# Kernel tuning notes

Measured on AMD Instinct MI355X. Metric: run time of the kernel, lower is better.

The kernel has to match this reference:

```python
import jax, jax.numpy as jnp
import numpy as np

N_NODES = 100000
DEG = 16
N_EDGES = N_NODES * DEG
D_FEAT = 64
HIDDEN = 64
K_RATIO = 0.5  # self.k
EPS = 1e-08


@jax.custom_vjp
def binary_step(x):
    return (x > 0.0).astype(x.dtype)

def _bs_fwd(x):
    return binary_step(x), x

def _bs_bwd(x, g):
    ax = jnp.abs(x)
    # BinaryStep surrogate gradient: 0 for |x|>1, 0.4 for 0.4<|x|<=1, else 2-4|x|
    add = jnp.where(ax > 1.0, 0.0, jnp.where(ax > 0.4, 0.4, 2.0 - 4.0 * ax))
    return (g * add,)

binary_step.defvjp(_bs_fwd, _bs_bwd)


def segment_softmax(v, seg, n):
    # torch.sparse.softmax(dim=1) == softmax over edges grouped by row id
    m = jax.ops.segment_max(v, seg, num_segments=n)
    e = jnp.exp(v - m[seg])
    s = jax.ops.segment_sum(e, seg, num_segments=n)
    return e / s[seg]


def setup_inputs() -> dict:
    key = jax.random.key(0)
    k1, k2, k3, k4, k5, k6, k7 = jax.random.split(key, 7)
    # coalesced edge list: rows sorted, (row,col) unique, every node has DEG edges
    rows = np.repeat(np.arange(N_NODES, dtype=np.int32), DEG)
    offs = np.tile(np.arange(1, DEG + 1, dtype=np.int32), N_NODES)
    cols = ((rows + offs) % N_NODES).reshape(N_NODES, DEG)
    cols = np.sort(cols, axis=1).reshape(-1).astype(np.int32)
    indices = jnp.asarray(np.stack([rows, cols]))  # [2, E]
    features = jax.random.normal(k1, (N_NODES, D_FEAT), dtype=jnp.float32)
    values = jax.random.uniform(k2, (N_EDGES,), dtype=jnp.float32, minval=0.1, maxval=1.0)
    U = jax.random.uniform(k3, (N_EDGES,), dtype=jnp.float32)
    gumbel = -jnp.log(-jnp.log(U + EPS) + EPS)  # Gumbel(0,1) noise (precomputed for determinism)
    in_dim = 2 * D_FEAT + 1
    w0 = jax.random.normal(k4, (HIDDEN, in_dim), dtype=jnp.float32) * (6.0 / (in_dim + HIDDEN)) ** 0.5
    b0 = jax.random.normal(k5, (HIDDEN,), dtype=jnp.float32) * 0.02
    w1 = jax.random.normal(k6, (1, HIDDEN), dtype=jnp.float32) * (6.0 / (HIDDEN + 1)) ** 0.5
    b1 = jax.random.normal(k7, (1,), dtype=jnp.float32) * 0.02
    return {"features": features, "values": values, "w0": w0, "b0": b0,
            "w1": w1, "b1": b1, "gumbel": gumbel, "indices": indices,
            "n_nodes": N_NODES, "temperature": 1}


def reference(features, values, w0, b0, w1, b1, gumbel, indices, n_nodes, temperature):
    rows = indices[0]
    cols = indices[1]
    # gather endpoint features + edge weight, 2-layer MLP -> scalar score per edge
    temp = jnp.concatenate([features[rows], features[cols], values[:, None]], axis=-1)  # [E, 2D+1]
    h = jax.nn.relu(temp @ w0.T + b0)          # [E, H]
    z = (h @ w1.T + b1).reshape(-1)            # [E]
    z = z / jnp.maximum(jnp.linalg.norm(z), 1e-12)  # F.normalize(dim=0)
    pi = segment_softmax(z, rows, n_nodes)           # sparse row softmax
    logits = (jnp.log(pi) + gumbel) / temperature    # gumbel_softmax_sample (training path)
    y = segment_softmax(logits, rows, n_nodes)
    # per-node top-k threshold masking
    counts = jax.ops.segment_sum(jnp.ones_like(rows), rows, num_segments=n_nodes)  # [N]
    k_edges = jnp.maximum(jnp.round(counts.astype(y.dtype) * K_RATIO).astype(rows.dtype), 1)
    val_sort_idx = jnp.argsort(-y)                                   # global descending sort
    idx_sort_idx = jnp.argsort(rows[val_sort_idx], stable=True)      # stable regroup by row
    scores_sorted = y[val_sort_idx][idx_sort_idx]                    # per-row descending scores
    rows_sorted = rows[val_sort_idx][idx_sort_idx]
    edge_start = jnp.concatenate([jnp.zeros((1,), counts.dtype), jnp.cumsum(counts[:-1])])
    edge_end = jnp.abs(edge_start + k_edges - 1)
    node_thre = scores_sorted[edge_end]          # k-th largest score per node
    thre_aug = node_thre[rows_sorted]            # == repeat_interleave(counts) since rows_sorted ascending
    mask = binary_step(scores_sorted - thre_aug + 1e-12)
    masked = mask * scores_sorted
    masked = masked[jnp.argsort(idx_sort_idx)]   # undo row regroup
    masked = masked[jnp.argsort(val_sort_idx)]   # undo value sort -> original edge order
    return masked
```

## Files before the change

### kernel.cpp

```cpp
#include <hip/hip_runtime.h>

#define N_NODES 100000
#define DEG 16
#define N_EDGES (N_NODES * DEG)
#define NT 64
#define NBLK2 ((N_NODES + NT - 1) / NT)
#define AB_TILES 2
#define NBLK_AB ((N_NODES + NT * AB_TILES - 1) / (NT * AB_TILES))

__global__ __launch_bounds__(256) void k_prep(const float* __restrict__ w0,
                                              float* __restrict__ w0T) {
    int id = blockIdx.x * 256 + threadIdx.x;
    if (id < 64 * 128) {
        int k = id >> 7, o = id & 127;
        w0T[k * 128 + o] = (o < 64) ? w0[o * 129 + k]
                                    : w0[(o - 64) * 129 + 64 + k];
    }
}

__global__ __launch_bounds__(256) void k_ab(const float* __restrict__ feat,
                                            const float* __restrict__ w0T,
                                            const float* __restrict__ b0,
                                            float* __restrict__ AB) {
    __shared__ float ws[64][128];
    __shared__ float fs[64][64];
    const int tid = threadIdx.x;
    const int to = tid & 31;
    const int tn = tid >> 5;

    for (int idx = tid; idx < 2048; idx += 256) {
        int k = idx >> 5, o4 = idx & 31;
        *(float4*)&ws[k][o4 * 4] = *(const float4*)&w0T[k * 128 + o4 * 4];
    }
    float4 bb = make_float4(0.f, 0.f, 0.f, 0.f);
    if (to < 16) bb = *(const float4*)(b0 + to * 4);

#define FMA16(ACCR, F4)                                   \
    ACCR[0] = fmaf(F4.x, w40.x, ACCR[0]);                 \
    ACCR[1] = fmaf(F4.x, w40.y, ACCR[1]);                 \
    ACCR[2] = fmaf(F4.x, w40.z, ACCR[2]);                 \
    ACCR[3] = fmaf(F4.x, w40.w, ACCR[3]);                 \
    ACCR[0] = fmaf(F4.y, w41.x, ACCR[0]);                 \
    ACCR[1] = fmaf(F4.y, w41.y, ACCR[1]);                 \
    ACCR[2] = fmaf(F4.y, w41.z, ACCR[2]);                 \
    ACCR[3] = fmaf(F4.y, w41.w, ACCR[3]);                 \
    ACCR[0] = fmaf(F4.z, w42.x, ACCR[0]);                 \
    ACCR[1] = fmaf(F4.z, w42.y, ACCR[1]);                 \
    ACCR[2] = fmaf(F4.z, w42.z, ACCR[2]);                 \
    ACCR[3] = fmaf(F4.z, w42.w, ACCR[3]);                 \
    ACCR[0] = fmaf(F4.w, w43.x, ACCR[0]);                 \
    ACCR[1] = fmaf(F4.w, w43.y, ACCR[1]);                 \
    ACCR[2] = fmaf(F4.w, w43.z, ACCR[2]);                 \
    ACCR[3] = fmaf(F4.w, w43.w, ACCR[3]);

#pragma unroll 1
    for (int tile = 0; tile < AB_TILES; ++tile) {
        const int n0 = blockIdx.x * (NT * AB_TILES) + tile * NT;
        if (n0 >= N_NODES) break;
        __syncthreads();
        for (int idx = tid; idx < 1024; idx += 256) {
            int flat = idx << 2;
            int nn = flat >> 6, k = flat & 63;
            int n = n0 + nn;
            float4 v = make_float4(0.f, 0.f, 0.f, 0.f);
            if (n < N_NODES) v = *(const float4*)(feat + (size_t)n * 64 + k);
            *(float4*)&fs[nn][k] = v;
        }
        __syncthreads();

        float acc[8][4];
#pragma unroll
        for (int a = 0; a < 8; ++a) {
            acc[a][0] = 0.f; acc[a][1] = 0.f; acc[a][2] = 0.f; acc[a][3] = 0.f;
        }
#pragma unroll 4
        for (int k4 = 0; k4 < 16; ++k4) {
            const int kk = k4 * 4;
            float4 w40 = *(const float4*)&ws[kk + 0][to * 4];
            float4 w41 = *(const float4*)&ws[kk + 1][to * 4];
            float4 w42 = *(const float4*)&ws[kk + 2][to * 4];
            float4 w43 = *(const float4*)&ws[kk + 3][to * 4];
#pragma unroll
            for (int a = 0; a < 8; ++a) {
                float4 f4 = *(const float4*)&fs[tn * 8 + a][kk];
                FMA16(acc[a], f4)
            }
        }
#pragma unroll
        for (int a = 0; a < 8; ++a) {
            int n = n0 + tn * 8 + a;
            if (n < N_NODES) {
                float4 o4 = make_float4(acc[a][0] + bb.x, acc[a][1] + bb.y,
                                        acc[a][2] + bb.z, acc[a][3] + bb.w);
                *(float4*)(AB + (size_t)n * 128 + to * 4) = o4;
            }
        }
    }
}

__global__ __launch_bounds__(256) void k_edge(const float* __restrict__ AB,
                                              const float* __restrict__ values,
                                              const int* __restrict__ indices,
                                              const float* __restrict__ w0,
                                              const float* __restrict__ w1,
                                              const float* __restrict__ b1,
                                              float* __restrict__ z,
                                              double* __restrict__ partial) {
    __shared__ float a_s[64][68];
    __shared__ float b_s[80][68];
    __shared__ float wv_s[64];
    __shared__ float w1_s[64];
    __shared__ double redw[4];
    const int t = threadIdx.x;
    const int n0 = blockIdx.x * NT;
    const int nvalid = min(NT, N_NODES - n0);

    if (t < 64) {
        wv_s[t] = w0[t * 129 + 128];
        w1_s[t] = w1[t];
    }
    for (int idx = t; idx < 1024; idx += 256) {
        int r = idx >> 4, k4 = idx & 15;
        float4 v = make_float4(0.f, 0.f, 0.f, 0.f);
        if (r < nvalid) v = *(const float4*)(AB + (size_t)(n0 + r) * 128 + k4 * 4);
        *(float4*)&a_s[r][k4 * 4] = v;
    }
    for (int idx = t; idx < 1280; idx += 256) {
        int r = idx >> 4, k4 = idx & 15;
        int node = n0 + 1 + r;
        if (node >= N_NODES) node -= N_NODES;
        *(float4*)&b_s[r][k4 * 4] = *(const float4*)(AB + (size_t)node * 128 + 64 + k4 * 4);
    }
    __syncthreads();

    const int row = t >> 2;
    const bool ok = row < nvalid;
    double ss = 0.0;
    if (ok) {
        const int ebase = n0 * 16 + (t << 2);
        int4   c4 = *(const int4*)(indices + N_EDGES + ebase);
        float4 v4 = *(const float4*)(values + ebase);
        int   cols[4] = {c4.x, c4.y, c4.z, c4.w};
        float vv[4]   = {v4.x, v4.y, v4.z, v4.w};
        int   ii[4];
        bool  fb[4];
        bool  anyfb = false;
#pragma unroll
        for (int k = 0; k < 4; ++k) {
            int i = cols[k] - (n0 + 1);
            if (i < 0) i += N_NODES;
            fb[k] = (i >= 80);
            anyfb |= fb[k];
            ii[k] = fb[k] ? 0 : i;
        }
        float acc[4] = {0.f, 0.f, 0.f, 0.f};
#pragma unroll
        for (int q = 0; q < 16; ++q) {
            float4 a4  = *(const float4*)&a_s[row][q * 4];
            float4 wv4 = *(const float4*)&wv_s[q * 4];
            float4 w14 = *(const float4*)&w1_s[q * 4];
#pragma unroll
            for (int k = 0; k < 4; ++k) {
                float4 b4 = *(const float4*)&b_s[ii[k]][q * 4];
                float t0 = fmaf(wv4.x, vv[k], a4.x + b4.x);
                float t1 = fmaf(wv4.y, vv[k], a4.y + b4.y);
                float t2 = fmaf(wv4.z, vv[k], a4.z + b4.z);
                float t3 = fmaf(wv4.w, vv[k], a4.w + b4.w);
                acc[k] = fmaf(w14.x, fmaxf(t0, 0.f), acc[k]);
                acc[k] = fmaf(w14.y, fmaxf(t1, 0.f), acc[k]);
                acc[k] = fmaf(w14.z, fmaxf(t2, 0.f), acc[k]);
                acc[k] = fmaf(w14.w, fmaxf(t3, 0.f), acc[k]);
            }
        }
        if (anyfb) {
#pragma unroll
            for (int k = 0; k < 4; ++k) {
                if (fb[k]) {
                    const float* Bp = AB + (size_t)cols[k] * 128 + 64;
                    float a = 0.f;
                    for (int h = 0; h < 64; ++h) {
                        float th = fmaf(wv_s[h], vv[k], a_s[row][h] + Bp[h]);
                        a = fmaf(w1_s[h], fmaxf(th, 0.f), a);
                    }
                    acc[k] = a;
                }
            }
        }
        const float b1v = b1[0];
        float4 z4;
        z4.x = acc[0] + b1v; z4.y = acc[1] + b1v;
        z4.z = acc[2] + b1v; z4.w = acc[3] + b1v;
        *(float4*)(z + ebase) = z4;
        ss = (double)z4.x * z4.x + (double)z4.y * z4.y +
             (double)z4.z * z4.z + (double)z4.w * z4.w;
    }
#pragma unroll
    for (int off = 32; off > 0; off >>= 1) ss += __shfl_down(ss, off, 64);
    if ((t & 63) == 0) redw[t >> 6] = ss;
    __syncthreads();
    if (t == 0) partial[blockIdx.x] = (redw[0] + redw[1]) + (redw[2] + redw[3]);
}

__global__ __launch_bounds__(256) void k_norm(const double* __restrict__ partial,
                                              double* __restrict__ nrm) {
    __shared__ double red[256];
    const int t = threadIdx.x;
    double s = 0.0;
    for (int i = t; i < NBLK2; i += 256) s += partial[i];
    red[t] = s;
    __syncthreads();
#pragma unroll
    for (int off = 128; off > 0; off >>= 1) {
        if (t < off) red[t] += red[t + off];
        __syncthreads();
    }
    if (t == 0) nrm[0] = fmax(sqrt(red[0]), 1e-12);
}

__global__ __launch_bounds__(256) void k_mask(const float* __restrict__ z,
                                              const float* __restrict__ gumbel,
                                              const double* __restrict__ nrm,
                                              const int* __restrict__ temperature,
                                              float* __restrict__ out) {
    const int n = blockIdx.x * 256 + threadIdx.x;
    if (n >= N_NODES) return;
    const double inv_nv = 1.0 / nrm[0];
    const double invT = 1.0 / (double)temperature[0];
    const float4* z4 = (const float4*)(z + (size_t)n * 16);
    const float4* g4 = (const float4*)(gumbel + (size_t)n * 16);
    double tl[16], y[16];
#pragma unroll
    for (int q = 0; q < 4; ++q) {
        float4 zv = z4[q];
        float4 gv = g4[q];
        tl[q * 4 + 0] = ((double)zv.x * inv_nv + (double)gv.x) * invT;
        tl[q * 4 + 1] = ((double)zv.y * inv_nv + (double)gv.y) * invT;
        tl[q * 4 + 2] = ((double)zv.z * inv_nv + (double)gv.z) * invT;
        tl[q * 4 + 3] = ((double)zv.w * inv_nv + (double)gv.w) * invT;
    }
    double m = tl[0];
#pragma unroll
    for (int i = 1; i < 16; ++i) m = fmax(m, tl[i]);
    double s = 0.0;
#pragma unroll
    for (int i = 0; i < 16; ++i) { y[i] = exp(tl[i] - m); s += y[i]; }
    const double inv_s = 1.0 / s;
#pragma unroll
    for (int i = 0; i < 16; ++i) y[i] *= inv_s;
    double thre = y[0];
#pragma unroll
    for (int i = 0; i < 16; ++i) {
        int c = 0, q = 0;
#pragma unroll
        for (int j = 0; j < 16; ++j) {
            c += (y[j] > y[i]) ? 1 : 0;
            q += (y[j] == y[i]) ? 1 : 0;
        }
        if (c <= 7 && 7 < c + q) thre = y[i];
    }
    float4* o4 = (float4*)(out + (size_t)n * 16);
#pragma unroll
    for (int qq = 0; qq < 4; ++qq) {
        float4 ov;
        ov.x = ((y[qq * 4 + 0] - thre + 1e-12) > 0.0) ? (float)y[qq * 4 + 0] : 0.f;
        ov.y = ((y[qq * 4 + 1] - thre + 1e-12) > 0.0) ? (float)y[qq * 4 + 1] : 0.f;
        ov.z = ((y[qq * 4 + 2] - thre + 1e-12) > 0.0) ? (float)y[qq * 4 + 2] : 0.f;
        ov.w = ((y[qq * 4 + 3] - thre + 1e-12) > 0.0) ? (float)y[qq * 4 + 3] : 0.f;
        o4[qq] = ov;
    }
}

extern "C" void kernel_launch(void* const* d_in, const int* in_sizes, int n_in,
                              void* d_out, int out_size, void* d_ws, size_t ws_size,
                              hipStream_t stream) {
    const float* feat    = (const float*)d_in[0];
    const float* values  = (const float*)d_in[1];
    const float* w0      = (const float*)d_in[2];
    const float* b0      = (const float*)d_in[3];
    const float* w1      = (const float*)d_in[4];
    const float* b1      = (const float*)d_in[5];
    const float* gumbel  = (const float*)d_in[6];
    const int*   indices = (const int*)d_in[7];
    const int*   temp    = (const int*)d_in[9];
    float* out = (float*)d_out;

    float*  w0T     = (float*)d_ws;
    float*  AB      = (float*)((char*)d_ws + 64 * 128 * 4);
    float*  zbuf    = (float*)((char*)d_ws + 64 * 128 * 4 + (size_t)N_NODES * 128 * 4);
    double* partial = (double*)((char*)d_ws + 64 * 128 * 4 + (size_t)N_NODES * 128 * 4
                                + (size_t)N_EDGES * 4);
    double* nrm     = partial + NBLK2;

    k_prep<<<32, 256, 0, stream>>>(w0, w0T);
    k_ab  <<<NBLK_AB, 256, 0, stream>>>(feat, w0T, b0, AB);
    k_edge<<<NBLK2, 256, 0, stream>>>(AB, values, indices, w0, w1, b1, zbuf, partial);
    k_norm<<<1, 256, 0, stream>>>(partial, nrm);
    k_mask<<<(N_NODES + 255) / 256, 256, 0, stream>>>(zbuf, gumbel, nrm, temp, out);
}
```

Baseline: 78.40 us.

## Retile node-projection GEMM to 8x8 per thread and read A rows directly

The k_ab projection kernel now processes 128 nodes per block in a single tile, with each thread computing an 8x8 output block instead of 8x4. The weight matrix is staged through LDS in two 32-row halves to keep shared memory small, and launch bounds request 3 blocks per CU. This raises FMA work per LDS load, at the cost of more registers and an extra sync. In k_edge the shared a_s staging is removed, and each thread reads its own node's A half directly from global memory, which cuts LDS use and a barrier-covered copy but puts uncoalesced per-thread global loads in the inner loop.

```diff
diff --git a/kernel.cpp b/kernel.cpp
--- a/kernel.cpp
+++ b/kernel.cpp
@@ -5,8 +5,8 @@
 #define N_EDGES (N_NODES * DEG)
 #define NT 64
 #define NBLK2 ((N_NODES + NT - 1) / NT)
-#define AB_TILES 2
-#define NBLK_AB ((N_NODES + NT * AB_TILES - 1) / (NT * AB_TILES))
+#define ABN 128
+#define NBLK_AB ((N_NODES + ABN - 1) / ABN)
 
 __global__ __launch_bounds__(256) void k_prep(const float* __restrict__ w0,
                                               float* __restrict__ w0T) {
@@ -18,82 +18,104 @@
     }
 }
 
-__global__ __launch_bounds__(256) void k_ab(const float* __restrict__ feat,
-                                            const float* __restrict__ w0T,
-                                            const float* __restrict__ b0,
-                                            float* __restrict__ AB) {
-    __shared__ float ws[64][128];
-    __shared__ float fs[64][64];
+__global__ __launch_bounds__(256, 3) void k_ab(const float* __restrict__ feat,
+                                               const float* __restrict__ w0T,
+                                               const float* __restrict__ b0,
+                                               float* __restrict__ AB) {
+    __shared__ float ws[32][128];
+    __shared__ float fs[128][64];
     const int tid = threadIdx.x;
-    const int to = tid & 31;
-    const int tn = tid >> 5;
+    const int n0 = blockIdx.x * ABN;
+    const int to = tid & 15;
+    const int tn = tid >> 4;
 
     for (int idx = tid; idx < 2048; idx += 256) {
-        int k = idx >> 5, o4 = idx & 31;
-        *(float4*)&ws[k][o4 * 4] = *(const float4*)&w0T[k * 128 + o4 * 4];
-    }
-    float4 bb = make_float4(0.f, 0.f, 0.f, 0.f);
-    if (to < 16) bb = *(const float4*)(b0 + to * 4);
-
-#define FMA16(ACCR, F4)                                   \
-    ACCR[0] = fmaf(F4.x, w40.x, ACCR[0]);                 \
-    ACCR[1] = fmaf(F4.x, w40.y, ACCR[1]);                 \
-    ACCR[2] = fmaf(F4.x, w40.z, ACCR[2]);                 \
-    ACCR[3] = fmaf(F4.x, w40.w, ACCR[3]);                 \
-    ACCR[0] = fmaf(F4.y, w41.x, ACCR[0]);                 \
-    ACCR[1] = fmaf(F4.y, w41.y, ACCR[1]);                 \
-    ACCR[2] = fmaf(F4.y, w41.z, ACCR[2]);                 \
-    ACCR[3] = fmaf(F4.y, w41.w, ACCR[3]);                 \
-    ACCR[0] = fmaf(F4.z, w42.x, ACCR[0]);                 \
-    ACCR[1] = fmaf(F4.z, w42.y, ACCR[1]);                 \
-    ACCR[2] = fmaf(F4.z, w42.z, ACCR[2]);                 \
-    ACCR[3] = fmaf(F4.z, w42.w, ACCR[3]);                 \
-    ACCR[0] = fmaf(F4.w, w43.x, ACCR[0]);                 \
-    ACCR[1] = fmaf(F4.w, w43.y, ACCR[1]);                 \
-    ACCR[2] = fmaf(F4.w, w43.z, ACCR[2]);                 \
-    ACCR[3] = fmaf(F4.w, w43.w, ACCR[3]);
+        int flat = idx << 2;
+        int nn = flat >> 6, k = flat & 63;
+        int n = n0 + nn;
+        float4 v = make_float4(0.f, 0.f, 0.f, 0.f);
+        if (n < N_NODES) v = *(const float4*)(feat + (size_t)n * 64 + k);
+        *(float4*)&fs[nn][k] = v;
+    }
+    for (int idx = tid; idx < 512; idx += 256) {
+        int k = idx >> 4, o4 = idx & 15;
+        *(float4*)&ws[k][o4 * 8] = *(const float4*)&w0T[k * 128 + o4 * 8];
+        *(float4*)&ws[k][o4 * 8 + 4] = *(const float4*)&w0T[k * 128 + o4 * 8 + 4];
+    }
+    __syncthreads();
+
+#define FMA16W(ACC, F4, W0, W1, W2, W3)                   \
+    ACC[0] = fmaf(F4.x, W0.x, ACC[0]);                    \
+    ACC[1] = fmaf(F4.x, W0.y, ACC[1]);                    \
+    ACC[2] = fmaf(F4.x, W0.z, ACC[2]);                    \
+    ACC[3] = fmaf(F4.x, W0.w, ACC[3]);                    \
+    ACC[0] = fmaf(F4.y, W1.x, ACC[0]);                    \
+    ACC[1] = fmaf(F4.y, W1.y, ACC[1]);                    \
+    ACC[2] = fmaf(F4.y, W1.z, ACC[2]);                    \
+    ACC[3] = fmaf(F4.y, W1.w, ACC[3]);                    \
+    ACC[0] = fmaf(F4.z, W2.x, ACC[0]);                    \
+    ACC[1] = fmaf(F4.z, W2.y, ACC[1]);                    \
+    ACC[2] = fmaf(F4.z, W2.z, ACC[2]);                    \
+    ACC[3] = fmaf(F4.z, W2.w, ACC[3]);                    \
+    ACC[0] = fmaf(F4.w, W3.x, ACC[0]);                    \
+    ACC[1] = fmaf(F4.w, W3.y, ACC[1]);                    \
+    ACC[2] = fmaf(F4.w, W3.z, ACC[2]);                    \
+    ACC[3] = fmaf(F4.w, W3.w, ACC[3]);
+
+    float acc[8][8];
+#pragma unroll
+    for (int a = 0; a < 8; ++a)
+#pragma unroll
+        for (int j = 0; j < 8; ++j) acc[a][j] = 0.f;
 
 #pragma unroll 1
-    for (int tile = 0; tile < AB_TILES; ++tile) {
-        const int n0 = blockIdx.x * (NT * AB_TILES) + tile * NT;
-        if (n0 >= N_NODES) break;
-        __syncthreads();
-        for (int idx = tid; idx < 1024; idx += 256) {
-            int flat = idx << 2;
-            int nn = flat >> 6, k = flat & 63;
-            int n = n0 + nn;
-            float4 v = make_float4(0.f, 0.f, 0.f, 0.f);
-            if (n < N_NODES) v = *(const float4*)(feat + (size_t)n * 64 + k);
-            *(float4*)&fs[nn][k] = v;
-        }
-        __syncthreads();
-
-        float acc[8][4];
-#pragma unroll
-        for (int a = 0; a < 8; ++a) {
-            acc[a][0] = 0.f; acc[a][1] = 0.f; acc[a][2] = 0.f; acc[a][3] = 0.f;
-        }
-#pragma unroll 4
-        for (int k4 = 0; k4 < 16; ++k4) {
+    for (int h = 0; h < 2; ++h) {
+        if (h == 1) {
+            __syncthreads();
+            for (int idx = tid; idx < 512; idx += 256) {
+                int k = idx >> 4, o4 = idx & 15;
+                *(float4*)&ws[k][o4 * 8] =
+                    *(const float4*)&w0T[(32 + k) * 128 + o4 * 8];
+                *(float4*)&ws[k][o4 * 8 + 4] =
+                    *(const float4*)&w0T[(32 + k) * 128 + o4 * 8 + 4];
+            }
+            __syncthreads();
+        }
+#pragma unroll
+        for (int k4 = 0; k4 < 8; ++k4) {
             const int kk = k4 * 4;
-            float4 w40 = *(const float4*)&ws[kk + 0][to * 4];
-            float4 w41 = *(const float4*)&ws[kk + 1][to * 4];
-            float4 w42 = *(const float4*)&ws[kk + 2][to * 4];
-            float4 w43 = *(const float4*)&ws[kk + 3][to * 4];
+            float4 w0a = *(const float4*)&ws[kk + 0][to * 8];
+            float4 w0b = *(const float4*)&ws[kk + 0][to * 8 + 4];
+            float4 w1a = *(const float4*)&ws[kk + 1][to * 8];
+            float4 w1b = *(const float4*)&ws[kk + 1][to * 8 + 4];
+            float4 w2a = *(const float4*)&ws[kk + 2][to * 8];
+            float4 w2b = *(const float4*)&ws[kk + 2][to * 8 + 4];
+            float4 w3a = *(const float4*)&ws[kk + 3][to * 8];
+            float4 w3b = *(const float4*)&ws[kk + 3][to * 8 + 4];
 #pragma unroll
             for (int a = 0; a < 8; ++a) {
-                float4 f4 = *(const float4*)&fs[tn * 8 + a][kk];
-                FMA16(acc[a], f4)
+                float4 f4 = *(const float4*)&fs[tn * 8 + a][h * 32 + kk];
+                FMA16W((acc[a] + 0), f4, w0a, w1a, w2a, w3a)
+                FMA16W((acc[a] + 4), f4, w0b, w1b, w2b, w3b)
             }
         }
-#pragma unroll
-        for (int a = 0; a < 8; ++a) {
-            int n = n0 + tn * 8 + a;
-            if (n < N_NODES) {
-                float4 o4 = make_float4(acc[a][0] + bb.x, acc[a][1] + bb.y,
-                                        acc[a][2] + bb.z, acc[a][3] + bb.w);
-                *(float4*)(AB + (size_t)n * 128 + to * 4) = o4;
-            }
+    }
+    float4 bba = make_float4(0.f, 0.f, 0.f, 0.f);
+    float4 bbb = make_float4(0.f, 0.f, 0.f, 0.f);
+    if (to < 8) {
+        bba = *(const float4*)(b0 + to * 8);
+        bbb = *(const float4*)(b0 + to * 8 + 4);
+    }
+#pragma unroll
+    for (int a = 0; a < 8; ++a) {
+        int n = n0 + tn * 8 + a;
+        if (n < N_NODES) {
+            float4 oa = make_float4(acc[a][0] + bba.x, acc[a][1] + bba.y,
+                                    acc[a][2] + bba.z, acc[a][3] + bba.w);
+            float4 ob = make_float4(acc[a][4] + bbb.x, acc[a][5] + bbb.y,
+                                    acc[a][6] + bbb.z, acc[a][7] + bbb.w);
+            *(float4*)(AB + (size_t)n * 128 + to * 8) = oa;
+            *(float4*)(AB + (size_t)n * 128 + to * 8 + 4) = ob;
         }
     }
 }
@@ -106,7 +128,6 @@
                                               const float* __restrict__ b1,
                                               float* __restrict__ z,
                                               double* __restrict__ partial) {
-    __shared__ float a_s[64][68];
     __shared__ float b_s[80][68];
     __shared__ float wv_s[64];
     __shared__ float w1_s[64];
@@ -119,12 +140,6 @@
         wv_s[t] = w0[t * 129 + 128];
         w1_s[t] = w1[t];
     }
-    for (int idx = t; idx < 1024; idx += 256) {
-        int r = idx >> 4, k4 = idx & 15;
-        float4 v = make_float4(0.f, 0.f, 0.f, 0.f);
-        if (r < nvalid) v = *(const float4*)(AB + (size_t)(n0 + r) * 128 + k4 * 4);
-        *(float4*)&a_s[r][k4 * 4] = v;
-    }
     for (int idx = t; idx < 1280; idx += 256) {
         int r = idx >> 4, k4 = idx & 15;
         int node = n0 + 1 + r;
@@ -137,6 +152,7 @@
     const bool ok = row < nvalid;
     double ss = 0.0;
     if (ok) {
+        const float* Ap = AB + (size_t)(n0 + row) * 128;
         const int ebase = n0 * 16 + (t << 2);
         int4   c4 = *(const int4*)(indices + N_EDGES + ebase);
         float4 v4 = *(const float4*)(values + ebase);
@@ -156,7 +172,7 @@
         float acc[4] = {0.f, 0.f, 0.f, 0.f};
 #pragma unroll
         for (int q = 0; q < 16; ++q) {
-            float4 a4  = *(const float4*)&a_s[row][q * 4];
+            float4 a4  = *(const float4*)(Ap + q * 4);
             float4 wv4 = *(const float4*)&wv_s[q * 4];
             float4 w14 = *(const float4*)&w1_s[q * 4];
 #pragma unroll
@@ -179,7 +195,7 @@
                     const float* Bp = AB + (size_t)cols[k] * 128 + 64;
                     float a = 0.f;
                     for (int h = 0; h < 64; ++h) {
-                        float th = fmaf(wv_s[h], vv[k], a_s[row][h] + Bp[h]);
+                        float th = fmaf(wv_s[h], vv[k], Ap[h] + Bp[h]);
                         a = fmaf(w1_s[h], fmaxf(th, 0.f), a);
                     }
                     acc[k] = a;
```

Result: slower. 117.0 us (+49.3%).

## Rewrite node projection as register-resident weights per wave; read A rows directly

Applied to the files above, without the earlier changes.

The projection kernel drops its shared-memory tiled GEMM. Each wave now keeps one 64-wide column slice of the transposed weight matrix in registers and walks 49 nodes two at a time, using wave-uniform feature loads that every lane reads. The edge kernel no longer stages the per-node A half in shared memory and reads it straight from global memory instead. This trades barriers and LDS traffic for heavy register use and redundant broadcast loads, which may lower occupancy.

```diff
diff --git a/kernel.cpp b/kernel.cpp
--- a/kernel.cpp
+++ b/kernel.cpp
@@ -5,8 +5,8 @@
 #define N_EDGES (N_NODES * DEG)
 #define NT 64
 #define NBLK2 ((N_NODES + NT - 1) / NT)
-#define AB_TILES 2
-#define NBLK_AB ((N_NODES + NT * AB_TILES - 1) / (NT * AB_TILES))
+#define NBLK_AB 1024
+#define NPW 49
 
 __global__ __launch_bounds__(256) void k_prep(const float* __restrict__ w0,
                                               float* __restrict__ w0T) {
@@ -22,80 +22,52 @@
                                             const float* __restrict__ w0T,
                                             const float* __restrict__ b0,
                                             float* __restrict__ AB) {
-    __shared__ float ws[64][128];
-    __shared__ float fs[64][64];
-    const int tid = threadIdx.x;
-    const int to = tid & 31;
-    const int tn = tid >> 5;
-
-    for (int idx = tid; idx < 2048; idx += 256) {
-        int k = idx >> 5, o4 = idx & 31;
-        *(float4*)&ws[k][o4 * 4] = *(const float4*)&w0T[k * 128 + o4 * 4];
-    }
-    float4 bb = make_float4(0.f, 0.f, 0.f, 0.f);
-    if (to < 16) bb = *(const float4*)(b0 + to * 4);
-
-#define FMA16(ACCR, F4)                                   \
-    ACCR[0] = fmaf(F4.x, w40.x, ACCR[0]);                 \
-    ACCR[1] = fmaf(F4.x, w40.y, ACCR[1]);                 \
-    ACCR[2] = fmaf(F4.x, w40.z, ACCR[2]);                 \
-    ACCR[3] = fmaf(F4.x, w40.w, ACCR[3]);                 \
-    ACCR[0] = fmaf(F4.y, w41.x, ACCR[0]);                 \
-    ACCR[1] = fmaf(F4.y, w41.y, ACCR[1]);                 \
-    ACCR[2] = fmaf(F4.y, w41.z, ACCR[2]);                 \
-    ACCR[3] = fmaf(F4.y, w41.w, ACCR[3]);                 \
-    ACCR[0] = fmaf(F4.z, w42.x, ACCR[0]);                 \
-    ACCR[1] = fmaf(F4.z, w42.y, ACCR[1]);                 \
-    ACCR[2] = fmaf(F4.z, w42.z, ACCR[2]);                 \
-    ACCR[3] = fmaf(F4.z, w42.w, ACCR[3]);                 \
-    ACCR[0] = fmaf(F4.w, w43.x, ACCR[0]);                 \
-    ACCR[1] = fmaf(F4.w, w43.y, ACCR[1]);                 \
-    ACCR[2] = fmaf(F4.w, w43.z, ACCR[2]);                 \
-    ACCR[3] = fmaf(F4.w, w43.w, ACCR[3]);
+    const int lane = threadIdx.x & 63;
+    const int wid  = threadIdx.x >> 6;
+    const int gw   = blockIdx.x * 4 + wid;
+    const int half = gw & 1;
+    const int wix  = gw >> 1;
+    const int start = wix * NPW;
+    if (start >= N_NODES) return;
+    const int lim = min(start + NPW, N_NODES);
+
+    float wreg[64];
+#pragma unroll
+    for (int k = 0; k < 64; ++k)
+        wreg[k] = w0T[k * 128 + half * 64 + lane];
+
+    const float b0v = (half == 0) ? b0[lane] : 0.f;
+
+#define FMA8(ACC, X, Y, KC)                                   \
+    ACC = fmaf(X.x, wreg[(KC) * 8 + 0], ACC);                 \
+    ACC = fmaf(X.y, wreg[(KC) * 8 + 1], ACC);                 \
+    ACC = fmaf(X.z, wreg[(KC) * 8 + 2], ACC);                 \
+    ACC = fmaf(X.w, wreg[(KC) * 8 + 3], ACC);                 \
+    ACC = fmaf(Y.x, wreg[(KC) * 8 + 4], ACC);                 \
+    ACC = fmaf(Y.y, wreg[(KC) * 8 + 5], ACC);                 \
+    ACC = fmaf(Y.z, wreg[(KC) * 8 + 6], ACC);                 \
+    ACC = fmaf(Y.w, wreg[(KC) * 8 + 7], ACC);
 
 #pragma unroll 1
-    for (int tile = 0; tile < AB_TILES; ++tile) {
-        const int n0 = blockIdx.x * (NT * AB_TILES) + tile * NT;
-        if (n0 >= N_NODES) break;
-        __syncthreads();
-        for (int idx = tid; idx < 1024; idx += 256) {
-            int flat = idx << 2;
-            int nn = flat >> 6, k = flat & 63;
-            int n = n0 + nn;
-            float4 v = make_float4(0.f, 0.f, 0.f, 0.f);
-            if (n < N_NODES) v = *(const float4*)(feat + (size_t)n * 64 + k);
-            *(float4*)&fs[nn][k] = v;
-        }
-        __syncthreads();
-
-        float acc[8][4];
-#pragma unroll
-        for (int a = 0; a < 8; ++a) {
-            acc[a][0] = 0.f; acc[a][1] = 0.f; acc[a][2] = 0.f; acc[a][3] = 0.f;
-        }
-#pragma unroll 4
-        for (int k4 = 0; k4 < 16; ++k4) {
-            const int kk = k4 * 4;
-            float4 w40 = *(const float4*)&ws[kk + 0][to * 4];
-            float4 w41 = *(const float4*)&ws[kk + 1][to * 4];
-            float4 w42 = *(const float4*)&ws[kk + 2][to * 4];
-            float4 w43 = *(const float4*)&ws[kk + 3][to * 4];
-#pragma unroll
-            for (int a = 0; a < 8; ++a) {
-                float4 f4 = *(const float4*)&fs[tn * 8 + a][kk];
-                FMA16(acc[a], f4)
-            }
-        }
-#pragma unroll
-        for (int a = 0; a < 8; ++a) {
-            int n = n0 + tn * 8 + a;
-            if (n < N_NODES) {
-                float4 o4 = make_float4(acc[a][0] + bb.x, acc[a][1] + bb.y,
-                                        acc[a][2] + bb.z, acc[a][3] + bb.w);
-                *(float4*)(AB + (size_t)n * 128 + to * 4) = o4;
-            }
-        }
-    }
+    for (int nb = start; nb < lim; nb += 2) {
+        const int n0u = __builtin_amdgcn_readfirstlane(nb);
+        const int n1u = __builtin_amdgcn_readfirstlane((nb + 1 < lim) ? nb + 1 : nb);
+        const float* f0 = feat + (size_t)n0u * 64;
+        const float* f1 = feat + (size_t)n1u * 64;
+        float a0 = 0.f, a1 = 0.f;
+#pragma unroll
+        for (int kc = 0; kc < 8; ++kc) {
+            float4 x0 = *(const float4*)(f0 + kc * 8);
+            float4 y0 = *(const float4*)(f0 + kc * 8 + 4);
+            float4 x1 = *(const float4*)(f1 + kc * 8);
+            float4 y1 = *(const float4*)(f1 + kc * 8 + 4);
+            FMA8(a0, x0, y0, kc)
+            FMA8(a1, x1, y1, kc)
+        }
+        AB[(size_t)n0u * 128 + half * 64 + lane] = a0 + b0v;
+        AB[(size_t)n1u * 128 + half * 64 + lane] = a1 + b0v;
+    }
+#undef FMA8
 }
 
 __global__ __launch_bounds__(256) void k_edge(const float* __restrict__ AB,
@@ -106,7 +78,6 @@
                                               const float* __restrict__ b1,
                                               float* __restrict__ z,
                                               double* __restrict__ partial) {
-    __shared__ float a_s[64][68];
     __shared__ float b_s[80][68];
     __shared__ float wv_s[64];
     __shared__ float w1_s[64];
@@ -119,12 +90,6 @@
         wv_s[t] = w0[t * 129 + 128];
         w1_s[t] = w1[t];
     }
-    for (int idx = t; idx < 1024; idx += 256) {
-        int r = idx >> 4, k4 = idx & 15;
-        float4 v = make_float4(0.f, 0.f, 0.f, 0.f);
-        if (r < nvalid) v = *(const float4*)(AB + (size_t)(n0 + r) * 128 + k4 * 4);
-        *(float4*)&a_s[r][k4 * 4] = v;
-    }
     for (int idx = t; idx < 1280; idx += 256) {
         int r = idx >> 4, k4 = idx & 15;
         int node = n0 + 1 + r;
@@ -137,6 +102,7 @@
     const bool ok = row < nvalid;
     double ss = 0.0;
     if (ok) {
+        const float* Ap = AB + (size_t)(n0 + row) * 128;
         const int ebase = n0 * 16 + (t << 2);
         int4   c4 = *(const int4*)(indices + N_EDGES + ebase);
         float4 v4 = *(const float4*)(values + ebase);
@@ -156,7 +122,7 @@
         float acc[4] = {0.f, 0.f, 0.f, 0.f};
 #pragma unroll
         for (int q = 0; q < 16; ++q) {
-            float4 a4  = *(const float4*)&a_s[row][q * 4];
+            float4 a4  = *(const float4*)(Ap + q * 4);
             float4 wv4 = *(const float4*)&wv_s[q * 4];
             float4 w14 = *(const float4*)&w1_s[q * 4];
 #pragma unroll
@@ -179,7 +145,7 @@
                     const float* Bp = AB + (size_t)cols[k] * 128 + 64;
                     float a = 0.f;
                     for (int h = 0; h < 64; ++h) {
-                        float th = fmaf(wv_s[h], vv[k], a_s[row][h] + Bp[h]);
+                        float th = fmaf(wv_s[h], vv[k], Ap[h] + Bp[h]);
                         a = fmaf(w1_s[h], fmaxf(th, 0.f), a);
                     }
                     acc[k] = a;
```

After: 87.93 us. 12.2% more time.
